# Performance work log

Measured on AMD Instinct MI355X. Metric: run time of the kernel, lower is better.

## Reference

```python
import jax, jax.numpy as jnp
import numpy as np

# Static multi-scale pyramid configuration (matches src_spatial_shapes / level_start_index inputs)
LEVEL_SHAPES = [(128, 128), (64, 64), (32, 32), (16, 16)]  # (H, W) per level
NH, NL, NP = 8, 4, 4  # n_heads, n_levels, n_points
D = 256


def setup_inputs() -> dict:
    key = jax.random.key(0)
    ks = jax.random.split(key, 24)
    N, Lq = 4, 8192
    Lin = sum(h * w for h, w in LEVEL_SHAPES)  # 21760
    d_ff = 4 * D
    inp = {
        "tgt": jax.random.normal(ks[0], (N, Lq, D), jnp.float32),
        "query_pos": jax.random.normal(ks[1], (N, Lq, D), jnp.float32),
        "reference_points": jax.random.uniform(ks[2], (N, Lq, NL, 2), jnp.float32),
        "src": jax.random.normal(ks[3], (N, Lin, D), jnp.float32),
        "src_spatial_shapes": jnp.array(LEVEL_SHAPES, dtype=jnp.int64),
        "level_start_index": jnp.array(np.cumsum([0] + [h * w for h, w in LEVEL_SHAPES[:-1]]), dtype=jnp.int64),
        "src_padding_mask": jnp.zeros((N, Lin), dtype=bool),
        # MSDeformAttn params
        "W_off": jax.random.normal(ks[4], (D, NH * NL * NP * 2), jnp.float32) * 0.01,
        "b_off": jax.random.normal(ks[5], (NH * NL * NP * 2,), jnp.float32) * 0.01,
        "W_attn": jax.random.normal(ks[6], (D, NH * NL * NP), jnp.float32) * 0.02,
        "b_attn": jnp.zeros((NH * NL * NP,), jnp.float32),
        "W_val": jax.random.normal(ks[7], (D, D), jnp.float32) * 0.02,
        "b_val": jnp.zeros((D,), jnp.float32),
        "W_out": jax.random.normal(ks[8], (D, D), jnp.float32) * 0.02,
        "b_out": jnp.zeros((D,), jnp.float32),
        # LN + MLP params
        "ln1_g": jnp.ones((D,), jnp.float32),
        "ln1_b": jnp.zeros((D,), jnp.float32),
        "W_fc1": jax.random.normal(ks[9], (D, d_ff), jnp.float32) * 0.02,
        "b_fc1": jnp.zeros((d_ff,), jnp.float32),
        "W_fc2": jax.random.normal(ks[10], (d_ff, D), jnp.float32) * 0.02,
        "b_fc2": jnp.zeros((D,), jnp.float32),
        "ln2_g": jnp.ones((D,), jnp.float32),
        "ln2_b": jnp.zeros((D,), jnp.float32),
    }
    return inp


def _layer_norm(x, g, b, eps=1e-5):
    x32 = x.astype(jnp.float32)
    m = x32.mean(-1, keepdims=True)
    v = x32.var(-1, keepdims=True)
    return (((x32 - m) * jax.lax.rsqrt(v + eps)) * g + b).astype(x.dtype)


def _sample_level(value_flat, H, W, loc):
    # value_flat: [N, H*W, NH, hd]; loc: [N, Lq, NH, NP, 2] in [0,1]
    # torch.grid_sample align_corners=False, padding_mode='zeros'
    x = loc[..., 0] * W - 0.5
    y = loc[..., 1] * H - 0.5
    x0 = jnp.floor(x)
    y0 = jnp.floor(y)
    dx, dy = x - x0, y - y0
    N, Lq, nh, P = x.shape
    hd = value_flat.shape[-1]
    corners = [
        (x0, y0, (1.0 - dx) * (1.0 - dy)),
        (x0 + 1.0, y0, dx * (1.0 - dy)),
        (x0, y0 + 1.0, (1.0 - dx) * dy),
        (x0 + 1.0, y0 + 1.0, dx * dy),
    ]
    out = jnp.zeros((N, Lq * P, nh, hd), value_flat.dtype)
    for cx, cy, w in corners:
        valid = (cx >= 0) & (cx <= W - 1) & (cy >= 0) & (cy <= H - 1)
        ix = jnp.clip(cx, 0, W - 1).astype(jnp.int32)
        iy = jnp.clip(cy, 0, H - 1).astype(jnp.int32)
        idx = (iy * W + ix).transpose(0, 1, 3, 2).reshape(N, Lq * P, nh)[..., None]
        v = jnp.take_along_axis(value_flat, idx, axis=1)  # [N, Lq*P, NH, hd]
        ww = (w * valid).transpose(0, 1, 3, 2).reshape(N, Lq * P, nh)[..., None]
        out = out + v * ww
    return out.reshape(N, Lq, P, nh, hd)  # [N, Lq, NP, NH, hd]


def reference(tgt, query_pos, reference_points, src, src_spatial_shapes,
              level_start_index, src_padding_mask,
              W_off, b_off, W_attn, b_attn, W_val, b_val, W_out, b_out,
              ln1_g, ln1_b, W_fc1, b_fc1, W_fc2, b_fc2, ln2_g, ln2_b):
    N, Lq, _ = tgt.shape
    hd = D // NH
    q = tgt + query_pos

    # value projection + padding mask
    value = src @ W_val + b_val
    value = jnp.where(src_padding_mask[..., None], 0.0, value)
    value = value.reshape(N, -1, NH, hd)

    # sampling offsets and attention weights
    off = (q @ W_off + b_off).reshape(N, Lq, NH, NL, NP, 2)
    aw = (q @ W_attn + b_attn).reshape(N, Lq, NH, NL * NP)
    aw = jax.nn.softmax(aw, axis=-1).reshape(N, Lq, NH, NL, NP)

    # normalize offsets by (W, H) per level
    normalizer = jnp.array([[w, h] for (h, w) in LEVEL_SHAPES], jnp.float32)  # [NL, 2]
    loc = reference_points[:, :, None, :, None, :] + off / normalizer[None, None, None, :, None, :]

    out = jnp.zeros((N, Lq, NH, hd), value.dtype)
    start = 0
    for l, (H, W) in enumerate(LEVEL_SHAPES):
        vflat = value[:, start:start + H * W]
        start += H * W
        sampled = _sample_level(vflat, H, W, loc[:, :, :, l])  # [N, Lq, NP, NH, hd]
        w_l = aw[:, :, :, l].transpose(0, 1, 3, 2)[..., None]  # [N, Lq, NP, NH, 1]
        out = out + (sampled * w_l).sum(axis=2)
    attn_out = out.reshape(N, Lq, D) @ W_out + b_out

    # residual + LN + MLP (named 'gelu' but is ReLU in source) + LN
    x = _layer_norm(tgt + attn_out, ln1_g, ln1_b)
    h = jax.nn.relu(x @ W_fc1 + b_fc1) @ W_fc2 + b_fc2
    x = _layer_norm(x + h, ln2_g, ln2_b)
    return x
```

## Files before the change

### kernel.cpp

```cpp
#include <hip/hip_runtime.h>
#include <hip/hip_bf16.h>

constexpr int NB    = 4;
constexpr int LQ    = 8192;
constexpr int DM    = 256;
constexpr int NHEAD = 8;
constexpr int HD    = 32;
constexpr int LIN   = 21760;
constexpr int DFF   = 1024;
constexpr int MQ    = NB * LQ;
constexpr int MV    = NB * LIN;

typedef __attribute__((ext_vector_type(8))) short short8;
typedef __attribute__((ext_vector_type(4))) float f32x4;

__device__ __forceinline__ ushort f2b(float f) {
  union { __hip_bfloat16 h; ushort u; } c;
  c.h = __float2bfloat16(f);
  return c.u;
}
__device__ __forceinline__ float b2f(ushort u) {
  return __uint_as_float((unsigned int)u << 16);
}

__device__ __forceinline__ void load_lds16(const ushort* g, ushort* l) {
  __builtin_amdgcn_global_load_lds(
      (const __attribute__((address_space(1))) void*)g,
      (__attribute__((address_space(3))) void*)l, 16, 0, 0);
}

__global__ __launch_bounds__(256) void k_packall(
    const float* __restrict__ Wval, const float* __restrict__ Woff,
    const float* __restrict__ Wattn, const float* __restrict__ Wout,
    const float* __restrict__ W1, const float* __restrict__ W2,
    ushort* __restrict__ wvalP, ushort* __restrict__ wqP,
    ushort* __restrict__ woutP, ushort* __restrict__ w1P,
    ushort* __restrict__ w2P) {
  const int bid = blockIdx.x;
  const float* W; ushort* P; int K, Nsrc, n_base, local;
  if (bid < 64)       { W = Wval;  P = wvalP; K = 256;  Nsrc = 256;  n_base = 0;   local = bid; }
  else if (bid < 128) { W = Woff;  P = wqP;   K = 256;  Nsrc = 256;  n_base = 0;   local = bid - 64; }
  else if (bid < 160) { W = Wattn; P = wqP;   K = 256;  Nsrc = 128;  n_base = 256; local = bid - 128; }
  else if (bid < 224) { W = Wout;  P = woutP; K = 256;  Nsrc = 256;  n_base = 0;   local = bid - 160; }
  else if (bid < 480) { W = W1;    P = w1P;   K = 256;  Nsrc = 1024; n_base = 0;   local = bid - 224; }
  else                { W = W2;    P = w2P;   K = 1024; Nsrc = 256;  n_base = 0;   local = bid - 480; }
  const int kb = local % (K >> 5), nb = local / (K >> 5);
  const int k0 = kb * 32, n0 = nb * 32;

  __shared__ float T[32][33];
  const int t = threadIdx.x;
  {
    const int r = t >> 3, c4 = t & 7;
    const float4 v = *reinterpret_cast<const float4*>(
        &W[(size_t)(k0 + r) * Nsrc + n0 + c4 * 4]);
    T[r][c4 * 4 + 0] = v.x;
    T[r][c4 * 4 + 1] = v.y;
    T[r][c4 * 4 + 2] = v.z;
    T[r][c4 * 4 + 3] = v.w;
  }
  __syncthreads();
  const int dn = t >> 3, q = t & 7;
  const int n = n_base + n0 + dn;
  const int k = k0 + q * 4;
  const int Tt = n >> 4, fr = n & 15, kg = (k >> 3) & 3;
  const int idx = Tt * (K >> 5) + (k >> 5);
  ushort4 o;
  o.x = f2b(T[q * 4 + 0][dn]);
  o.y = f2b(T[q * 4 + 1][dn]);
  o.z = f2b(T[q * 4 + 2][dn]);
  o.w = f2b(T[q * 4 + 3][dn]);
  *reinterpret_cast<ushort4*>(&P[(size_t)idx * 512 + (kg * 16 + fr) * 8 + (k & 7)]) = o;
}

template<int MODE, int ASRC>
__global__ __launch_bounds__(256) void k_gemm(
    const void* __restrict__ Ap, const float* __restrict__ A2,
    const ushort* __restrict__ BP,
    const float* __restrict__ bias,
    void* __restrict__ out0, int M, int N, int K) {
  __shared__ __align__(16) ushort SMEM[17408];
  ushort* As = SMEM;
  const int m0 = blockIdx.x * 128, n0 = blockIdx.y * 128;
  const int t = threadIdx.x, w = t >> 6, l = t & 63;
  const int wr = (w >> 1) * 64, wc = (w & 1) * 64;
  const int fr = l & 15, kg = l >> 4;
  const int lrow = l >> 3;
  const int sg = (l & 7) ^ lrow;
  const int Kg = K >> 5;

  f32x4 acc[4][4];
#pragma unroll
  for (int i = 0; i < 4; ++i)
#pragma unroll
    for (int j = 0; j < 4; ++j) acc[i][j] = f32x4{0.f, 0.f, 0.f, 0.f};

  const float* Af = (const float*)Ap;

  for (int k0 = 0; k0 < K; k0 += 64) {
    float4 fa[4][2];
#pragma unroll
    for (int i = 0; i < 4; ++i) {
      const float* ap = Af + (size_t)(m0 + i * 32 + w * 8 + lrow) * K + k0 + sg * 8;
      fa[i][0] = *reinterpret_cast<const float4*>(ap);
      fa[i][1] = *reinterpret_cast<const float4*>(ap + 4);
      if constexpr (ASRC == 2) {
        const float* ap2 = A2 + (size_t)(m0 + i * 32 + w * 8 + lrow) * K + k0 + sg * 8;
        const float4 x = *reinterpret_cast<const float4*>(ap2);
        const float4 y = *reinterpret_cast<const float4*>(ap2 + 4);
        fa[i][0].x += x.x; fa[i][0].y += x.y; fa[i][0].z += x.z; fa[i][0].w += x.w;
        fa[i][1].x += y.x; fa[i][1].y += y.y; fa[i][1].z += y.z; fa[i][1].w += y.w;
      }
    }
    __syncthreads();
#pragma unroll
    for (int i = 0; i < 4; ++i) {
      uint4 u;
      u.x = (unsigned int)f2b(fa[i][0].x) | ((unsigned int)f2b(fa[i][0].y) << 16);
      u.y = (unsigned int)f2b(fa[i][0].z) | ((unsigned int)f2b(fa[i][0].w) << 16);
      u.z = (unsigned int)f2b(fa[i][1].x) | ((unsigned int)f2b(fa[i][1].y) << 16);
      u.w = (unsigned int)f2b(fa[i][1].z) | ((unsigned int)f2b(fa[i][1].w) << 16);
      *reinterpret_cast<uint4*>(As + i * 2048 + w * 512 + l * 8) = u;
    }
    __syncthreads();
#pragma unroll
    for (int kk = 0; kk < 2; ++kk) {
      short8 a[4], b[4];
#pragma unroll
      for (int i = 0; i < 4; ++i)
        a[i] = *reinterpret_cast<const short8*>(
            &As[(wr + i * 16 + fr) * 64 + ((kk * 4 + kg) ^ (fr & 7)) * 8]);
#pragma unroll
      for (int i = 0; i < 4; ++i)
        b[i] = *reinterpret_cast<const short8*>(
            BP + ((size_t)((n0 >> 4) + (w & 1) * 4 + i) * Kg + (k0 >> 5) + kk) * 512 + l * 8);
#pragma unroll
      for (int mi = 0; mi < 4; ++mi)
#pragma unroll
        for (int ni = 0; ni < 4; ++ni)
          acc[mi][ni] = __builtin_amdgcn_mfma_f32_16x16x32_bf16(
              b[ni], a[mi], acc[mi][ni], 0, 0, 0);
    }
  }

  ushort (*LC)[136] = (ushort(*)[136])SMEM;
  __syncthreads();
#pragma unroll
  for (int ni = 0; ni < 4; ++ni) {
    const float4 bv = *reinterpret_cast<const float4*>(&bias[n0 + wc + ni * 16 + kg * 4]);
#pragma unroll
    for (int mi = 0; mi < 4; ++mi) {
      ushort4 p;
      p.x = f2b(acc[mi][ni][0] + bv.x);
      p.y = f2b(acc[mi][ni][1] + bv.y);
      p.z = f2b(acc[mi][ni][2] + bv.z);
      p.w = f2b(acc[mi][ni][3] + bv.w);
      *reinterpret_cast<ushort4*>(&LC[wr + mi * 16 + fr][wc + ni * 16 + kg * 4]) = p;
    }
  }
  __syncthreads();
  const int c = t & 15, rb = t >> 4;
#pragma unroll
  for (int i = 0; i < 8; ++i) {
    const int r = rb + i * 16;
    const uint4 vv = *reinterpret_cast<const uint4*>(&LC[r][c * 8]);
    *reinterpret_cast<uint4*>((ushort*)out0 + (size_t)(m0 + r) * N + n0 + c * 8) = vv;
  }
}

__global__ __launch_bounds__(256) void k_qlogit(
    const float* __restrict__ tgt, const float* __restrict__ qpos,
    const ushort* __restrict__ BP, const float* __restrict__ battn,
    float* __restrict__ awb) {
  __shared__ __align__(16) ushort SMEM[17408];
  ushort* As = SMEM;
  const int m0 = blockIdx.x * 128;
  const int t = threadIdx.x, w = t >> 6, l = t & 63;
  const int wc = (w & 1) * 64;
  const int fr = l & 15, kg = l >> 4;
  const int lrow = l >> 3;
  const int sg = (l & 7) ^ lrow;

  f32x4 acc[4][4];
#pragma unroll
  for (int i = 0; i < 4; ++i)
#pragma unroll
    for (int j = 0; j < 4; ++j) acc[i][j] = f32x4{0.f, 0.f, 0.f, 0.f};

  for (int k0 = 0; k0 < 256; k0 += 64) {
    float4 fa[4][2];
#pragma unroll
    for (int i = 0; i < 4; ++i) {
      const float* ap = tgt + (size_t)(m0 + i * 32 + w * 8 + lrow) * 256 + k0 + sg * 8;
      const float* ap2 = qpos + (size_t)(m0 + i * 32 + w * 8 + lrow) * 256 + k0 + sg * 8;
      fa[i][0] = *reinterpret_cast<const float4*>(ap);
      fa[i][1] = *reinterpret_cast<const float4*>(ap + 4);
      const float4 x = *reinterpret_cast<const float4*>(ap2);
      const float4 y = *reinterpret_cast<const float4*>(ap2 + 4);
      fa[i][0].x += x.x; fa[i][0].y += x.y; fa[i][0].z += x.z; fa[i][0].w += x.w;
      fa[i][1].x += y.x; fa[i][1].y += y.y; fa[i][1].z += y.z; fa[i][1].w += y.w;
    }
    __syncthreads();
#pragma unroll
    for (int i = 0; i < 4; ++i) {
      uint4 u;
      u.x = (unsigned int)f2b(fa[i][0].x) | ((unsigned int)f2b(fa[i][0].y) << 16);
      u.y = (unsigned int)f2b(fa[i][0].z) | ((unsigned int)f2b(fa[i][0].w) << 16);
      u.z = (unsigned int)f2b(fa[i][1].x) | ((unsigned int)f2b(fa[i][1].y) << 16);
      u.w = (unsigned int)f2b(fa[i][1].z) | ((unsigned int)f2b(fa[i][1].w) << 16);
      *reinterpret_cast<uint4*>(As + i * 2048 + w * 512 + l * 8) = u;
    }
    __syncthreads();
#pragma unroll
    for (int kk = 0; kk < 2; ++kk) {
      short8 a[4], b[4];
#pragma unroll
      for (int i = 0; i < 4; ++i)
        a[i] = *reinterpret_cast<const short8*>(
            &As[((w >> 1) * 64 + i * 16 + fr) * 64 + ((kk * 4 + kg) ^ (fr & 7)) * 8]);
#pragma unroll
      for (int i = 0; i < 4; ++i)
        b[i] = *reinterpret_cast<const short8*>(
            BP + ((size_t)(16 + (w & 1) * 4 + i) * 8 + (k0 >> 5) + kk) * 512 + l * 8);
#pragma unroll
      for (int mi = 0; mi < 4; ++mi)
#pragma unroll
        for (int ni = 0; ni < 4; ++ni)
          acc[mi][ni] = __builtin_amdgcn_mfma_f32_16x16x32_bf16(
              b[ni], a[mi], acc[mi][ni], 0, 0, 0);
    }
  }

  float (*LF)[132] = (float(*)[132])SMEM;
#pragma unroll
  for (int p = 0; p < 2; ++p) {
    __syncthreads();
    if ((w >> 1) == p) {
#pragma unroll
      for (int ni = 0; ni < 4; ++ni) {
        const float4 bv = *reinterpret_cast<const float4*>(&battn[wc + ni * 16 + kg * 4]);
#pragma unroll
        for (int mi = 0; mi < 4; ++mi) {
          float4 v;
          v.x = acc[mi][ni][0] + bv.x; v.y = acc[mi][ni][1] + bv.y;
          v.z = acc[mi][ni][2] + bv.z; v.w = acc[mi][ni][3] + bv.w;
          *reinterpret_cast<float4*>(&LF[mi * 16 + fr][wc + ni * 16 + kg * 4]) = v;
        }
      }
    }
    __syncthreads();
#pragma unroll
    for (int gi = 0; gi < 2; ++gi) {
      const int g = t + gi * 256;
      const int row = g >> 3, hh = g & 7;
      const float* src = &LF[row][hh * 16];
      float e[16];
      float4 v0 = *reinterpret_cast<const float4*>(src);
      float4 v1 = *reinterpret_cast<const float4*>(src + 4);
      float4 v2 = *reinterpret_cast<const float4*>(src + 8);
      float4 v3 = *reinterpret_cast<const float4*>(src + 12);
      e[0]=v0.x; e[1]=v0.y; e[2]=v0.z; e[3]=v0.w;
      e[4]=v1.x; e[5]=v1.y; e[6]=v1.z; e[7]=v1.w;
      e[8]=v2.x; e[9]=v2.y; e[10]=v2.z; e[11]=v2.w;
      e[12]=v3.x; e[13]=v3.y; e[14]=v3.z; e[15]=v3.w;
      float mx = e[0];
#pragma unroll
      for (int i = 1; i < 16; ++i) mx = fmaxf(mx, e[i]);
      float s = 0.f;
#pragma unroll
      for (int i = 0; i < 16; ++i) { e[i] = __expf(e[i] - mx); s += e[i]; }
      const float inv = 1.f / s;
      float* o = awb + (size_t)(m0 + p * 64 + row) * 128 + hh * 16;
      float4 q;
      q.x = e[0]*inv; q.y = e[1]*inv; q.z = e[2]*inv; q.w = e[3]*inv;
      *reinterpret_cast<float4*>(o) = q;
      q.x = e[4]*inv; q.y = e[5]*inv; q.z = e[6]*inv; q.w = e[7]*inv;
      *reinterpret_cast<float4*>(o + 4) = q;
      q.x = e[8]*inv; q.y = e[9]*inv; q.z = e[10]*inv; q.w = e[11]*inv;
      *reinterpret_cast<float4*>(o + 8) = q;
      q.x = e[12]*inv; q.y = e[13]*inv; q.z = e[14]*inv; q.w = e[15]*inv;
      *reinterpret_cast<float4*>(o + 12) = q;
    }
  }
}

__global__ __launch_bounds__(256) void k_outln(
    const ushort* __restrict__ A, const ushort* __restrict__ BP,
    const float* __restrict__ bias, const float* __restrict__ res,
    const float* __restrict__ g, const float* __restrict__ bvec,
    ushort* __restrict__ out, int K) {
  __shared__ __align__(16) ushort SMEM[17408];
  ushort* As = SMEM;
  const int m0 = blockIdx.x * 64;
  const int t = threadIdx.x, w = t >> 6, l = t & 63;
  const int wc = w * 64;
  const int fr = l & 15, kg = l >> 4;
  const int lrow = l >> 3;
  const int sg = (l & 7) ^ lrow;
  const int Kg = K >> 5;

  f32x4 acc[4][4];
#pragma unroll
  for (int i = 0; i < 4; ++i)
#pragma unroll
    for (int j = 0; j < 4; ++j) acc[i][j] = f32x4{0.f, 0.f, 0.f, 0.f};

  for (int k0 = 0; k0 < K; k0 += 64) {
    __syncthreads();
#pragma unroll
    for (int i = 0; i < 2; ++i)
      load_lds16(A + (size_t)(m0 + i * 32 + w * 8 + lrow) * K + k0 + sg * 8,
                 As + i * 2048 + w * 512);
    __syncthreads();
#pragma unroll
    for (int kk = 0; kk < 2; ++kk) {
      short8 a[4], b[4];
#pragma unroll
      for (int i = 0; i < 4; ++i)
        a[i] = *reinterpret_cast<const short8*>(
            &As[(i * 16 + fr) * 64 + ((kk * 4 + kg) ^ (fr & 7)) * 8]);
#pragma unroll
      for (int i = 0; i < 4; ++i)
        b[i] = *reinterpret_cast<const short8*>(
            BP + ((size_t)(w * 4 + i) * Kg + (k0 >> 5) + kk) * 512 + l * 8);
#pragma unroll
      for (int mi = 0; mi < 4; ++mi)
#pragma unroll
        for (int ni = 0; ni < 4; ++ni)
          acc[mi][ni] = __builtin_amdgcn_mfma_f32_16x16x32_bf16(
              b[ni], a[mi], acc[mi][ni], 0, 0, 0);
    }
  }

  ushort (*LY)[272] = (ushort(*)[272])SMEM;
  __syncthreads();
#pragma unroll
  for (int ni = 0; ni < 4; ++ni) {
    const float4 bv = *reinterpret_cast<const float4*>(&bias[wc + ni * 16 + kg * 4]);
#pragma unroll
    for (int mi = 0; mi < 4; ++mi) {
      ushort4 p;
      p.x = f2b(acc[mi][ni][0] + bv.x);
      p.y = f2b(acc[mi][ni][1] + bv.y);
      p.z = f2b(acc[mi][ni][2] + bv.z);
      p.w = f2b(acc[mi][ni][3] + bv.w);
      *reinterpret_cast<ushort4*>(&LY[mi * 16 + fr][wc + ni * 16 + kg * 4]) = p;
    }
  }
  __syncthreads();

  const int c = t & 31, rb = t >> 5;
#pragma unroll
  for (int i = 0; i < 8; ++i) {
    const int r = rb + i * 8;
    const uint4 yy = *reinterpret_cast<const uint4*>(&LY[r][c * 8]);
    const unsigned int yw[4] = {yy.x, yy.y, yy.z, yy.w};
    float v[8];
#pragma unroll
    for (int j = 0; j < 4; ++j) {
      v[2 * j]     = __uint_as_float(yw[j] << 16);
      v[2 * j + 1] = __uint_as_float(yw[j] & 0xffff0000u);
    }
    const float* rp = res + (size_t)(m0 + r) * 256 + c * 8;
    const float4 r0 = *reinterpret_cast<const float4*>(rp);
    const float4 r1 = *reinterpret_cast<const float4*>(rp + 4);
    v[0] += r0.x; v[1] += r0.y; v[2] += r0.z; v[3] += r0.w;
    v[4] += r1.x; v[5] += r1.y; v[6] += r1.z; v[7] += r1.w;
    float s = 0.f, ss = 0.f;
#pragma unroll
    for (int j = 0; j < 8; ++j) { s += v[j]; ss += v[j] * v[j]; }
#pragma unroll
    for (int o = 1; o < 32; o <<= 1) {
      s  += __shfl_xor(s, o);
      ss += __shfl_xor(ss, o);
    }
    const float m = s * (1.f / 256.f);
    const float inv = rsqrtf(ss * (1.f / 256.f) - m * m + 1e-5f);
    const float4 g0 = *reinterpret_cast<const float4*>(&g[c * 8]);
    const float4 g1 = *reinterpret_cast<const float4*>(&g[c * 8 + 4]);
    const float4 b0 = *reinterpret_cast<const float4*>(&bvec[c * 8]);
    const float4 b1 = *reinterpret_cast<const float4*>(&bvec[c * 8 + 4]);
    uint4 u;
    u.x = (unsigned int)f2b((v[0] - m) * inv * g0.x + b0.x) |
          ((unsigned int)f2b((v[1] - m) * inv * g0.y + b0.y) << 16);
    u.y = (unsigned int)f2b((v[2] - m) * inv * g0.z + b0.z) |
          ((unsigned int)f2b((v[3] - m) * inv * g0.w + b0.w) << 16);
    u.z = (unsigned int)f2b((v[4] - m) * inv * g1.x + b1.x) |
          ((unsigned int)f2b((v[5] - m) * inv * g1.y + b1.y) << 16);
    u.w = (unsigned int)f2b((v[6] - m) * inv * g1.z + b1.z) |
          ((unsigned int)f2b((v[7] - m) * inv * g1.w + b1.w) << 16);
    *reinterpret_cast<uint4*>(out + (size_t)(m0 + r) * 256 + c * 8) = u;
  }
}

__global__ __launch_bounds__(256) void k_ffn(
    const ushort* __restrict__ X, const ushort* __restrict__ W1P,
    const float* __restrict__ bb1, const ushort* __restrict__ W2P,
    const float* __restrict__ bb2, const float* __restrict__ g2,
    const float* __restrict__ b2v, float* __restrict__ out) {
  __shared__ __align__(16) ushort SMEM[24576];
  ushort* Xs = SMEM;
  ushort* Hs = SMEM + 16384;
  const int m0 = blockIdx.x * 64;
  const int t = threadIdx.x, w = t >> 6, l = t & 63;
  const int fr = l & 15, kg = l >> 4;

#pragma unroll
  for (int i = 0; i < 8; ++i) {
    const int gi = w * 8 + i;
    const int row = gi * 2 + (l >> 5);
    load_lds16(X + (size_t)(m0 + row) * 256 + (((l & 31) ^ (row & 7)) * 8),
               Xs + gi * 512);
  }
  __syncthreads();

  f32x4 acc2[4][4];
#pragma unroll
  for (int i = 0; i < 4; ++i)
#pragma unroll
    for (int j = 0; j < 4; ++j) acc2[i][j] = f32x4{0.f, 0.f, 0.f, 0.f};

  for (int c = 0; c < 8; ++c) {
    f32x4 acc1[4][2];
#pragma unroll
    for (int i = 0; i < 4; ++i)
#pragma unroll
      for (int j = 0; j < 2; ++j) acc1[i][j] = f32x4{0.f, 0.f, 0.f, 0.f};
#pragma unroll
    for (int ks = 0; ks < 8; ++ks) {
      short8 a[4], b[2];
#pragma unroll
      for (int mi = 0; mi < 4; ++mi)
        a[mi] = *reinterpret_cast<const short8*>(
            &Xs[(mi * 16 + fr) * 256 + ((ks * 4 + kg) ^ (fr & 7)) * 8]);
#pragma unroll
      for (int ni = 0; ni < 2; ++ni)
        b[ni] = *reinterpret_cast<const short8*>(
            W1P + ((size_t)(c * 8 + w * 2 + ni) * 8 + ks) * 512 + l * 8);
#pragma unroll
      for (int mi = 0; mi < 4; ++mi)
#pragma unroll
        for (int ni = 0; ni < 2; ++ni)
          acc1[mi][ni] = __builtin_amdgcn_mfma_f32_16x16x32_bf16(
              b[ni], a[mi], acc1[mi][ni], 0, 0, 0);
    }
    __syncthreads();
#pragma unroll
    for (int ni = 0; ni < 2; ++ni) {
      const float4 bv = *reinterpret_cast<const float4*>(
          &bb1[c * 128 + w * 32 + ni * 16 + kg * 4]);
#pragma unroll
      for (int mi = 0; mi < 4; ++mi) {
        const int row = mi * 16 + fr;
        const int gcol = w * 4 + ni * 2 + (kg >> 1);
        ushort4 p;
        p.x = f2b(fmaxf(acc1[mi][ni][0] + bv.x, 0.f));
        p.y = f2b(fmaxf(acc1[mi][ni][1] + bv.y, 0.f));
        p.z = f2b(fmaxf(acc1[mi][ni][2] + bv.z, 0.f));
        p.w = f2b(fmaxf(acc1[mi][ni][3] + bv.w, 0.f));
        *reinterpret_cast<ushort4*>(
            &Hs[row * 128 + ((gcol ^ (fr & 7)) * 8) + (kg & 1) * 4]) = p;
      }
    }
    __syncthreads();
#pragma unroll
    for (int ks2 = 0; ks2 < 4; ++ks2) {
      short8 a2[4], b2[4];
#pragma unroll
      for (int mi = 0; mi < 4; ++mi)
        a2[mi] = *reinterpret_cast<const short8*>(
            &Hs[(mi * 16 + fr) * 128 + ((ks2 * 4 + kg) ^ (fr & 7)) * 8]);
#pragma unroll
      for (int ni = 0; ni < 4; ++ni)
        b2[ni] = *reinterpret_cast<const short8*>(
            W2P + ((size_t)(w * 4 + ni) * 32 + c * 4 + ks2) * 512 + l * 8);
#pragma unroll
      for (int mi = 0; mi < 4; ++mi)
#pragma unroll
        for (int ni = 0; ni < 4; ++ni)
          acc2[mi][ni] = __builtin_amdgcn_mfma_f32_16x16x32_bf16(
              b2[ni], a2[mi], acc2[mi][ni], 0, 0, 0);
    }
  }

#pragma unroll
  for (int ni = 0; ni < 4; ++ni) {
    const int colb = w * 64 + ni * 16 + kg * 4;
    const float4 bv = *reinterpret_cast<const float4*>(&bb2[colb]);
    const int g = w * 8 + ni * 2 + (kg >> 1);
#pragma unroll
    for (int mi = 0; mi < 4; ++mi) {
      const int row = mi * 16 + fr;
      const ushort4 xr = *reinterpret_cast<const ushort4*>(
          &Xs[row * 256 + ((g ^ (fr & 7)) * 8) + (kg & 1) * 4]);
      acc2[mi][ni][0] += bv.x + b2f(xr.x);
      acc2[mi][ni][1] += bv.y + b2f(xr.y);
      acc2[mi][ni][2] += bv.z + b2f(xr.z);
      acc2[mi][ni][3] += bv.w + b2f(xr.w);
    }
  }
  __syncthreads();

  ushort (*LY)[272] = (ushort(*)[272])SMEM;
#pragma unroll
  for (int ni = 0; ni < 4; ++ni) {
#pragma unroll
    for (int mi = 0; mi < 4; ++mi) {
      ushort4 p;
      p.x = f2b(acc2[mi][ni][0]);
      p.y = f2b(acc2[mi][ni][1]);
      p.z = f2b(acc2[mi][ni][2]);
      p.w = f2b(acc2[mi][ni][3]);
      *reinterpret_cast<ushort4*>(&LY[mi * 16 + fr][w * 64 + ni * 16 + kg * 4]) = p;
    }
  }
  __syncthreads();

  const int cc = t & 31, rb = t >> 5;
#pragma unroll
  for (int i = 0; i < 8; ++i) {
    const int r = rb + i * 8;
    const uint4 yy = *reinterpret_cast<const uint4*>(&LY[r][cc * 8]);
    const unsigned int yw[4] = {yy.x, yy.y, yy.z, yy.w};
    float v[8];
#pragma unroll
    for (int j = 0; j < 4; ++j) {
      v[2 * j]     = __uint_as_float(yw[j] << 16);
      v[2 * j + 1] = __uint_as_float(yw[j] & 0xffff0000u);
    }
    float s = 0.f, ss = 0.f;
#pragma unroll
    for (int j = 0; j < 8; ++j) { s += v[j]; ss += v[j] * v[j]; }
#pragma unroll
    for (int o = 1; o < 32; o <<= 1) {
      s  += __shfl_xor(s, o);
      ss += __shfl_xor(ss, o);
    }
    const float m = s * (1.f / 256.f);
    const float inv = rsqrtf(ss * (1.f / 256.f) - m * m + 1e-5f);
    const float4 g0 = *reinterpret_cast<const float4*>(&g2[cc * 8]);
    const float4 g1 = *reinterpret_cast<const float4*>(&g2[cc * 8 + 4]);
    const float4 b0 = *reinterpret_cast<const float4*>(&b2v[cc * 8]);
    const float4 b1 = *reinterpret_cast<const float4*>(&b2v[cc * 8 + 4]);
    float* opp = out + (size_t)(m0 + r) * 256 + cc * 8;
    float4 q0, q1;
    q0.x = (v[0] - m) * inv * g0.x + b0.x;
    q0.y = (v[1] - m) * inv * g0.y + b0.y;
    q0.z = (v[2] - m) * inv * g0.z + b0.z;
    q0.w = (v[3] - m) * inv * g0.w + b0.w;
    q1.x = (v[4] - m) * inv * g1.x + b1.x;
    q1.y = (v[5] - m) * inv * g1.y + b1.y;
    q1.z = (v[6] - m) * inv * g1.z + b1.z;
    q1.w = (v[7] - m) * inv * g1.w + b1.w;
    *reinterpret_cast<float4*>(opp) = q0;
    *reinterpret_cast<float4*>(opp + 4) = q1;
  }
}

__global__ __launch_bounds__(256) void k_sample(
    const float* __restrict__ refp, const ushort* __restrict__ offb,
    const float* __restrict__ awb, const ushort* __restrict__ value,
    ushort* __restrict__ pre) {
  const int bid = ((blockIdx.x & 7) << 9) | (blockIdx.x >> 3);
  const int tid = bid * 256 + threadIdx.x;
  const int cg = tid & 3;
  const int h  = (tid >> 2) & 7;
  const int nq = tid >> 5;
  const int n  = nq >> 13;

  const float4 r01 = *reinterpret_cast<const float4*>(refp + (size_t)nq * 8);
  const float4 r23 = *reinterpret_cast<const float4*>(refp + (size_t)nq * 8 + 4);
  const float rxs[4] = {r01.x, r01.z, r23.x, r23.z};
  const float rys[4] = {r01.y, r01.w, r23.y, r23.w};
  const ushort* op = offb + (size_t)nq * 256 + h * 32;
  const float*  ap = awb + (size_t)nq * 128 + h * 16;
  const ushort* vb = value + (size_t)n * LIN * DM + h * HD + cg * 8;

  float acc[8];
#pragma unroll
  for (int j = 0; j < 8; ++j) acc[j] = 0.f;

  const int WL[4] = {128, 64, 32, 16};
  const int ST[4] = {0, 16384, 20480, 21504};

#pragma unroll
  for (int lvl = 0; lvl < 4; ++lvl) {
    const int Wl = WL[lvl];
    const float fW = (float)Wl;
    const float invW = 1.f / fW;
    const float rx = rxs[lvl], ry = rys[lvl];
    const ushort* vl = vb + (size_t)ST[lvl] * DM;
    const uint4 ov = *reinterpret_cast<const uint4*>(op + lvl * 8);
    const float4 a4 = *reinterpret_cast<const float4*>(ap + lvl * 4);
    const unsigned int ow[4] = {ov.x, ov.y, ov.z, ov.w};
    const float aa[4] = {a4.x, a4.y, a4.z, a4.w};
#pragma unroll
    for (int p = 0; p < 4; ++p) {
      const float ox = __uint_as_float(ow[p] << 16);
      const float oy = __uint_as_float(ow[p] & 0xffff0000u);
      const float xx = (rx + ox * invW) * fW - 0.5f;
      const float yy = (ry + oy * invW) * fW - 0.5f;
      const float a = aa[p];
      const float x0 = floorf(xx), y0 = floorf(yy);
      const float dx = xx - x0, dy = yy - y0;
      const bool vx0 = (x0 >= 0.f) && (x0 <= fW - 1.f);
      const bool vx1 = (x0 + 1.f >= 0.f) && (x0 + 1.f <= fW - 1.f);
      const bool vy0 = (y0 >= 0.f) && (y0 <= fW - 1.f);
      const bool vy1 = (y0 + 1.f >= 0.f) && (y0 + 1.f <= fW - 1.f);
      const int ix0 = min(max((int)x0, 0), Wl - 1);
      const int ix1 = min(max((int)x0 + 1, 0), Wl - 1);
      const int iy0 = min(max((int)y0, 0), Wl - 1);
      const int iy1 = min(max((int)y0 + 1, 0), Wl - 1);
      const float w00 = (vx0 && vy0) ? (1.f - dx) * (1.f - dy) * a : 0.f;
      const float w10 = (vx1 && vy0) ? dx * (1.f - dy) * a : 0.f;
      const float w01 = (vx0 && vy1) ? (1.f - dx) * dy * a : 0.f;
      const float w11 = (vx1 && vy1) ? dx * dy * a : 0.f;
      const ushort* r0 = vl + (size_t)iy0 * Wl * DM;
      const ushort* r1 = vl + (size_t)iy1 * Wl * DM;
      const uint4 u00 = *reinterpret_cast<const uint4*>(r0 + ix0 * DM);
      const uint4 u10 = *reinterpret_cast<const uint4*>(r0 + ix1 * DM);
      const uint4 u01 = *reinterpret_cast<const uint4*>(r1 + ix0 * DM);
      const uint4 u11 = *reinterpret_cast<const uint4*>(r1 + ix1 * DM);
      const unsigned int uu00[4] = {u00.x, u00.y, u00.z, u00.w};
      const unsigned int uu10[4] = {u10.x, u10.y, u10.z, u10.w};
      const unsigned int uu01[4] = {u01.x, u01.y, u01.z, u01.w};
      const unsigned int uu11[4] = {u11.x, u11.y, u11.z, u11.w};
#pragma unroll
      for (int i = 0; i < 4; ++i) {
        acc[2 * i]     += __uint_as_float(uu00[i] << 16) * w00;
        acc[2 * i + 1] += __uint_as_float(uu00[i] & 0xffff0000u) * w00;
        acc[2 * i]     += __uint_as_float(uu10[i] << 16) * w10;
        acc[2 * i + 1] += __uint_as_float(uu10[i] & 0xffff0000u) * w10;
        acc[2 * i]     += __uint_as_float(uu01[i] << 16) * w01;
        acc[2 * i + 1] += __uint_as_float(uu01[i] & 0xffff0000u) * w01;
        acc[2 * i]     += __uint_as_float(uu11[i] << 16) * w11;
        acc[2 * i + 1] += __uint_as_float(uu11[i] & 0xffff0000u) * w11;
      }
    }
  }

  uint4 o;
  o.x = (unsigned int)f2b(acc[0]) | ((unsigned int)f2b(acc[1]) << 16);
  o.y = (unsigned int)f2b(acc[2]) | ((unsigned int)f2b(acc[3]) << 16);
  o.z = (unsigned int)f2b(acc[4]) | ((unsigned int)f2b(acc[5]) << 16);
  o.w = (unsigned int)f2b(acc[6]) | ((unsigned int)f2b(acc[7]) << 16);
  *reinterpret_cast<uint4*>(pre + (size_t)nq * DM + h * HD + cg * 8) = o;
}

extern "C" void kernel_launch(void* const* d_in, const int* in_sizes, int n_in,
                              void* d_out, int out_size, void* d_ws, size_t ws_size,
                              hipStream_t stream) {
  const float* tgt   = (const float*)d_in[0];
  const float* qpos  = (const float*)d_in[1];
  const float* refp  = (const float*)d_in[2];
  const float* src   = (const float*)d_in[3];
  const float* Woff  = (const float*)d_in[7];
  const float* boff  = (const float*)d_in[8];
  const float* Wattn = (const float*)d_in[9];
  const float* battn = (const float*)d_in[10];
  const float* Wval  = (const float*)d_in[11];
  const float* bval  = (const float*)d_in[12];
  const float* Wout  = (const float*)d_in[13];
  const float* bout  = (const float*)d_in[14];
  const float* g1    = (const float*)d_in[15];
  const float* b1    = (const float*)d_in[16];
  const float* W1    = (const float*)d_in[17];
  const float* bb1   = (const float*)d_in[18];
  const float* W2    = (const float*)d_in[19];
  const float* bb2   = (const float*)d_in[20];
  const float* g2    = (const float*)d_in[21];
  const float* b2v   = (const float*)d_in[22];
  float* out = (float*)d_out;

  char* ws = (char*)d_ws;
  ushort* offb   = (ushort*)(ws + 0);
  ushort* valueb = (ushort*)(ws + 44564480);
  ushort* preb   = (ushort*)(ws + 89128960);
  float*  awb    = (float*)(ws + 105906176);
  ushort* xb     = (ushort*)(ws + 0);
  ushort* wvalP  = (ushort*)(ws + 156237824);
  ushort* wqP    = wvalP + 65536;
  ushort* woutP  = wqP + 98304;
  ushort* w1P    = woutP + 65536;
  ushort* w2P    = w1P + 262144;

  hipLaunchKernelGGL(k_packall, dim3(736), dim3(256), 0, stream,
                     Wval, Woff, Wattn, Wout, W1, W2,
                     wvalP, wqP, woutP, w1P, w2P);

  hipLaunchKernelGGL((k_gemm<0, 1>), dim3(MV / 128, 2), dim3(256), 0, stream,
                     (const void*)src, (const float*)nullptr, wvalP, bval,
                     (void*)valueb, MV, DM, DM);

  hipLaunchKernelGGL((k_gemm<0, 2>), dim3(MQ / 128, 2), dim3(256), 0, stream,
                     (const void*)tgt, qpos, wqP, boff,
                     (void*)offb, MQ, DM, DM);

  hipLaunchKernelGGL(k_qlogit, dim3(MQ / 128), dim3(256), 0, stream,
                     tgt, qpos, wqP, battn, awb);

  hipLaunchKernelGGL(k_sample, dim3(MQ * NHEAD * 4 / 256), dim3(256), 0, stream,
                     refp, offb, awb, valueb, preb);

  hipLaunchKernelGGL(k_outln, dim3(MQ / 64), dim3(256), 0, stream,
                     preb, woutP, bout, tgt, g1, b1, xb, DM);

  hipLaunchKernelGGL(k_ffn, dim3(MQ / 64), dim3(256), 0, stream,
                     xb, w1P, bb1, w2P, bb2, g2, b2v, out);
}
```

Measured before the change: 219.9 us.

## Store value tensor head-major and remap sampler blocks to one head per block

The value-projection GEMM gets a new output mode that writes the value tensor as [N, head, pixel, 32] instead of [N, pixel, 256], so each head's pixels sit contiguously. The sampling kernel is remapped so each block handles 64 queries of a single (batch, head) pair, and bilinear gathers index into the compact per-head plane. This aims to improve cache locality for the random bilinear gathers, since one block now only touches that head's slice of the value tensor. The GEMM epilogue gains per-row division and scattered 16-byte stores, and the adjacent-thread access pattern in the sampler changes.

```diff
diff --git a/kernel.cpp b/kernel.cpp
--- a/kernel.cpp
+++ b/kernel.cpp
@@ -163,7 +163,17 @@
   for (int i = 0; i < 8; ++i) {
     const int r = rb + i * 16;
     const uint4 vv = *reinterpret_cast<const uint4*>(&LC[r][c * 8]);
-    *reinterpret_cast<uint4*>((ushort*)out0 + (size_t)(m0 + r) * N + n0 + c * 8) = vv;
+    if constexpr (MODE == 0) {
+      *reinterpret_cast<uint4*>((ushort*)out0 + (size_t)(m0 + r) * N + n0 + c * 8) = vv;
+    } else {
+      const int row = m0 + r;
+      const int n = row / LIN;
+      const int pix = row - n * LIN;
+      const int col = n0 + c * 8;
+      const int h = col >> 5, ch = col & 31;
+      *reinterpret_cast<uint4*>((ushort*)out0 +
+          (((size_t)(n * NHEAD + h) * LIN + pix) * 32 + ch)) = vv;
+    }
   }
 }
 
@@ -560,12 +570,12 @@
     const float* __restrict__ refp, const ushort* __restrict__ offb,
     const float* __restrict__ awb, const ushort* __restrict__ value,
     ushort* __restrict__ pre) {
-  const int bid = ((blockIdx.x & 7) << 9) | (blockIdx.x >> 3);
-  const int tid = bid * 256 + threadIdx.x;
-  const int cg = tid & 3;
-  const int h  = (tid >> 2) & 7;
-  const int nq = tid >> 5;
-  const int n  = nq >> 13;
+  const int work = ((blockIdx.x & 7) << 9) | (blockIdx.x >> 3);
+  const int nh = work >> 7;
+  const int n = nh >> 3, h = nh & 7;
+  const int t = threadIdx.x;
+  const int cg = t & 3, qi = t >> 2;
+  const int nq = n * LQ + (work & 127) * 64 + qi;
 
   const float4 r01 = *reinterpret_cast<const float4*>(refp + (size_t)nq * 8);
   const float4 r23 = *reinterpret_cast<const float4*>(refp + (size_t)nq * 8 + 4);
@@ -573,7 +583,7 @@
   const float rys[4] = {r01.y, r01.w, r23.y, r23.w};
   const ushort* op = offb + (size_t)nq * 256 + h * 32;
   const float*  ap = awb + (size_t)nq * 128 + h * 16;
-  const ushort* vb = value + (size_t)n * LIN * DM + h * HD + cg * 8;
+  const ushort* vb = value + (size_t)nh * LIN * 32 + cg * 8;
 
   float acc[8];
 #pragma unroll
@@ -588,7 +598,7 @@
     const float fW = (float)Wl;
     const float invW = 1.f / fW;
     const float rx = rxs[lvl], ry = rys[lvl];
-    const ushort* vl = vb + (size_t)ST[lvl] * DM;
+    const ushort* vl = vb + (size_t)ST[lvl] * 32;
     const uint4 ov = *reinterpret_cast<const uint4*>(op + lvl * 8);
     const float4 a4 = *reinterpret_cast<const float4*>(ap + lvl * 4);
     const unsigned int ow[4] = {ov.x, ov.y, ov.z, ov.w};
@@ -614,12 +624,12 @@
       const float w10 = (vx1 && vy0) ? dx * (1.f - dy) * a : 0.f;
       const float w01 = (vx0 && vy1) ? (1.f - dx) * dy * a : 0.f;
       const float w11 = (vx1 && vy1) ? dx * dy * a : 0.f;
-      const ushort* r0 = vl + (size_t)iy0 * Wl * DM;
-      const ushort* r1 = vl + (size_t)iy1 * Wl * DM;
-      const uint4 u00 = *reinterpret_cast<const uint4*>(r0 + ix0 * DM);
-      const uint4 u10 = *reinterpret_cast<const uint4*>(r0 + ix1 * DM);
-      const uint4 u01 = *reinterpret_cast<const uint4*>(r1 + ix0 * DM);
-      const uint4 u11 = *reinterpret_cast<const uint4*>(r1 + ix1 * DM);
+      const ushort* r0 = vl + (size_t)iy0 * Wl * 32;
+      const ushort* r1 = vl + (size_t)iy1 * Wl * 32;
+      const uint4 u00 = *reinterpret_cast<const uint4*>(r0 + ix0 * 32);
+      const uint4 u10 = *reinterpret_cast<const uint4*>(r0 + ix1 * 32);
+      const uint4 u01 = *reinterpret_cast<const uint4*>(r1 + ix0 * 32);
+      const uint4 u11 = *reinterpret_cast<const uint4*>(r1 + ix1 * 32);
       const unsigned int uu00[4] = {u00.x, u00.y, u00.z, u00.w};
       const unsigned int uu10[4] = {u10.x, u10.y, u10.z, u10.w};
       const unsigned int uu01[4] = {u01.x, u01.y, u01.z, u01.w};
@@ -643,7 +653,7 @@
   o.y = (unsigned int)f2b(acc[2]) | ((unsigned int)f2b(acc[3]) << 16);
   o.z = (unsigned int)f2b(acc[4]) | ((unsigned int)f2b(acc[5]) << 16);
   o.w = (unsigned int)f2b(acc[6]) | ((unsigned int)f2b(acc[7]) << 16);
-  *reinterpret_cast<uint4*>(pre + (size_t)nq * DM + h * HD + cg * 8) = o;
+  *reinterpret_cast<uint4*>(pre + (size_t)nq * 256 + h * 32 + cg * 8) = o;
 }
 
 extern "C" void kernel_launch(void* const* d_in, const int* in_sizes, int n_in,
@@ -687,7 +697,7 @@
                      Wval, Woff, Wattn, Wout, W1, W2,
                      wvalP, wqP, woutP, w1P, w2P);
 
-  hipLaunchKernelGGL((k_gemm<0, 1>), dim3(MV / 128, 2), dim3(256), 0, stream,
+  hipLaunchKernelGGL((k_gemm<4, 1>), dim3(MV / 128, 2), dim3(256), 0, stream,
                      (const void*)src, (const float*)nullptr, wvalP, bval,
                      (void*)valueb, MV, DM, DM);
 
```

After: 242.3 us. +10.2%, slower.

## Fuse sampling-offset GEMM and attention-logit softmax into one query projection kernel

Applied to the files above, without the earlier changes.

Replaces the separate offset GEMM and attention-logit kernel with a single kernel that computes all 384 output columns (256 offsets plus 128 logits) from one load of tgt+query_pos per 64-row tile. Each wave handles 96 columns, and the epilogue writes the bf16 offsets and a softmaxed weight buffer in three staged passes through shared memory. This removes a second read of tgt and qpos and one launch. In exchange, the logits are now rounded to bf16 before the softmax, which slightly reduces their precision, and the kernel holds a larger per-thread accumulator set.

```diff
diff --git a/kernel.cpp b/kernel.cpp
--- a/kernel.cpp
+++ b/kernel.cpp
@@ -72,12 +72,10 @@
   *reinterpret_cast<ushort4*>(&P[(size_t)idx * 512 + (kg * 16 + fr) * 8 + (k & 7)]) = o;
 }
 
-template<int MODE, int ASRC>
-__global__ __launch_bounds__(256) void k_gemm(
-    const void* __restrict__ Ap, const float* __restrict__ A2,
-    const ushort* __restrict__ BP,
+__global__ __launch_bounds__(256) void k_gemmA(
+    const float* __restrict__ Af, const ushort* __restrict__ BP,
     const float* __restrict__ bias,
-    void* __restrict__ out0, int M, int N, int K) {
+    ushort* __restrict__ out0, int M, int N, int K) {
   __shared__ __align__(16) ushort SMEM[17408];
   ushort* As = SMEM;
   const int m0 = blockIdx.x * 128, n0 = blockIdx.y * 128;
@@ -94,8 +92,6 @@
 #pragma unroll
     for (int j = 0; j < 4; ++j) acc[i][j] = f32x4{0.f, 0.f, 0.f, 0.f};
 
-  const float* Af = (const float*)Ap;
-
   for (int k0 = 0; k0 < K; k0 += 64) {
     float4 fa[4][2];
 #pragma unroll
@@ -103,13 +99,6 @@
       const float* ap = Af + (size_t)(m0 + i * 32 + w * 8 + lrow) * K + k0 + sg * 8;
       fa[i][0] = *reinterpret_cast<const float4*>(ap);
       fa[i][1] = *reinterpret_cast<const float4*>(ap + 4);
-      if constexpr (ASRC == 2) {
-        const float* ap2 = A2 + (size_t)(m0 + i * 32 + w * 8 + lrow) * K + k0 + sg * 8;
-        const float4 x = *reinterpret_cast<const float4*>(ap2);
-        const float4 y = *reinterpret_cast<const float4*>(ap2 + 4);
-        fa[i][0].x += x.x; fa[i][0].y += x.y; fa[i][0].z += x.z; fa[i][0].w += x.w;
-        fa[i][1].x += y.x; fa[i][1].y += y.y; fa[i][1].z += y.z; fa[i][1].w += y.w;
-      }
     }
     __syncthreads();
 #pragma unroll
@@ -163,35 +152,37 @@
   for (int i = 0; i < 8; ++i) {
     const int r = rb + i * 16;
     const uint4 vv = *reinterpret_cast<const uint4*>(&LC[r][c * 8]);
-    *reinterpret_cast<uint4*>((ushort*)out0 + (size_t)(m0 + r) * N + n0 + c * 8) = vv;
-  }
-}
-
-__global__ __launch_bounds__(256) void k_qlogit(
+    *reinterpret_cast<uint4*>(out0 + (size_t)(m0 + r) * N + n0 + c * 8) = vv;
+  }
+}
+
+__global__ __launch_bounds__(256) void k_qproj(
     const float* __restrict__ tgt, const float* __restrict__ qpos,
-    const ushort* __restrict__ BP, const float* __restrict__ battn,
-    float* __restrict__ awb) {
-  __shared__ __align__(16) ushort SMEM[17408];
+    const ushort* __restrict__ BP, const float* __restrict__ boff,
+    const float* __restrict__ battn,
+    ushort* __restrict__ offb, float* __restrict__ awb) {
+  __shared__ __align__(16) ushort SMEM[8704];
+  __shared__ __align__(16) ushort LY[64][136];
   ushort* As = SMEM;
-  const int m0 = blockIdx.x * 128;
+  const int m0 = blockIdx.x * 64;
   const int t = threadIdx.x, w = t >> 6, l = t & 63;
-  const int wc = (w & 1) * 64;
   const int fr = l & 15, kg = l >> 4;
   const int lrow = l >> 3;
   const int sg = (l & 7) ^ lrow;
 
-  f32x4 acc[4][4];
+  f32x4 acc[4][6];
 #pragma unroll
   for (int i = 0; i < 4; ++i)
 #pragma unroll
-    for (int j = 0; j < 4; ++j) acc[i][j] = f32x4{0.f, 0.f, 0.f, 0.f};
+    for (int j = 0; j < 6; ++j) acc[i][j] = f32x4{0.f, 0.f, 0.f, 0.f};
 
   for (int k0 = 0; k0 < 256; k0 += 64) {
-    float4 fa[4][2];
-#pragma unroll
-    for (int i = 0; i < 4; ++i) {
-      const float* ap = tgt + (size_t)(m0 + i * 32 + w * 8 + lrow) * 256 + k0 + sg * 8;
-      const float* ap2 = qpos + (size_t)(m0 + i * 32 + w * 8 + lrow) * 256 + k0 + sg * 8;
+    float4 fa[2][2];
+#pragma unroll
+    for (int i = 0; i < 2; ++i) {
+      const int row = m0 + i * 32 + w * 8 + lrow;
+      const float* ap = tgt + (size_t)row * 256 + k0 + sg * 8;
+      const float* ap2 = qpos + (size_t)row * 256 + k0 + sg * 8;
       fa[i][0] = *reinterpret_cast<const float4*>(ap);
       fa[i][1] = *reinterpret_cast<const float4*>(ap + 4);
       const float4 x = *reinterpret_cast<const float4*>(ap2);
@@ -201,7 +192,7 @@
     }
     __syncthreads();
 #pragma unroll
-    for (int i = 0; i < 4; ++i) {
+    for (int i = 0; i < 2; ++i) {
       uint4 u;
       u.x = (unsigned int)f2b(fa[i][0].x) | ((unsigned int)f2b(fa[i][0].y) << 16);
       u.y = (unsigned int)f2b(fa[i][0].z) | ((unsigned int)f2b(fa[i][0].w) << 16);
@@ -212,73 +203,86 @@
     __syncthreads();
 #pragma unroll
     for (int kk = 0; kk < 2; ++kk) {
-      short8 a[4], b[4];
+      short8 a[4], b[6];
 #pragma unroll
       for (int i = 0; i < 4; ++i)
         a[i] = *reinterpret_cast<const short8*>(
-            &As[((w >> 1) * 64 + i * 16 + fr) * 64 + ((kk * 4 + kg) ^ (fr & 7)) * 8]);
-#pragma unroll
-      for (int i = 0; i < 4; ++i)
+            &As[(i * 16 + fr) * 64 + ((kk * 4 + kg) ^ (fr & 7)) * 8]);
+#pragma unroll
+      for (int i = 0; i < 6; ++i)
         b[i] = *reinterpret_cast<const short8*>(
-            BP + ((size_t)(16 + (w & 1) * 4 + i) * 8 + (k0 >> 5) + kk) * 512 + l * 8);
+            BP + ((size_t)(w * 6 + i) * 8 + (k0 >> 5) + kk) * 512 + l * 8);
 #pragma unroll
       for (int mi = 0; mi < 4; ++mi)
 #pragma unroll
-        for (int ni = 0; ni < 4; ++ni)
+        for (int ni = 0; ni < 6; ++ni)
           acc[mi][ni] = __builtin_amdgcn_mfma_f32_16x16x32_bf16(
               b[ni], a[mi], acc[mi][ni], 0, 0, 0);
     }
   }
 
-  float (*LF)[132] = (float(*)[132])SMEM;
-#pragma unroll
-  for (int p = 0; p < 2; ++p) {
-    __syncthreads();
-    if ((w >> 1) == p) {
-#pragma unroll
-      for (int ni = 0; ni < 4; ++ni) {
-        const float4 bv = *reinterpret_cast<const float4*>(&battn[wc + ni * 16 + kg * 4]);
+#pragma unroll
+  for (int p = 0; p < 3; ++p) {
+    __syncthreads();
+#pragma unroll
+    for (int ni = 0; ni < 6; ++ni) {
+      const int cb = w * 96 + ni * 16;
+      if (cb >= p * 128 && cb < p * 128 + 128) {
+        const int col = cb + kg * 4;
+        float4 bv;
+        if (col < 256) bv = *reinterpret_cast<const float4*>(&boff[col]);
+        else           bv = *reinterpret_cast<const float4*>(&battn[col - 256]);
 #pragma unroll
         for (int mi = 0; mi < 4; ++mi) {
-          float4 v;
-          v.x = acc[mi][ni][0] + bv.x; v.y = acc[mi][ni][1] + bv.y;
-          v.z = acc[mi][ni][2] + bv.z; v.w = acc[mi][ni][3] + bv.w;
-          *reinterpret_cast<float4*>(&LF[mi * 16 + fr][wc + ni * 16 + kg * 4]) = v;
+          ushort4 q;
+          q.x = f2b(acc[mi][ni][0] + bv.x);
+          q.y = f2b(acc[mi][ni][1] + bv.y);
+          q.z = f2b(acc[mi][ni][2] + bv.z);
+          q.w = f2b(acc[mi][ni][3] + bv.w);
+          *reinterpret_cast<ushort4*>(&LY[mi * 16 + fr][cb - p * 128 + kg * 4]) = q;
         }
       }
     }
     __syncthreads();
-#pragma unroll
-    for (int gi = 0; gi < 2; ++gi) {
-      const int g = t + gi * 256;
-      const int row = g >> 3, hh = g & 7;
-      const float* src = &LF[row][hh * 16];
-      float e[16];
-      float4 v0 = *reinterpret_cast<const float4*>(src);
-      float4 v1 = *reinterpret_cast<const float4*>(src + 4);
-      float4 v2 = *reinterpret_cast<const float4*>(src + 8);
-      float4 v3 = *reinterpret_cast<const float4*>(src + 12);
-      e[0]=v0.x; e[1]=v0.y; e[2]=v0.z; e[3]=v0.w;
-      e[4]=v1.x; e[5]=v1.y; e[6]=v1.z; e[7]=v1.w;
-      e[8]=v2.x; e[9]=v2.y; e[10]=v2.z; e[11]=v2.w;
-      e[12]=v3.x; e[13]=v3.y; e[14]=v3.z; e[15]=v3.w;
-      float mx = e[0];
-#pragma unroll
-      for (int i = 1; i < 16; ++i) mx = fmaxf(mx, e[i]);
-      float s = 0.f;
-#pragma unroll
-      for (int i = 0; i < 16; ++i) { e[i] = __expf(e[i] - mx); s += e[i]; }
-      const float inv = 1.f / s;
-      float* o = awb + (size_t)(m0 + p * 64 + row) * 128 + hh * 16;
-      float4 q;
-      q.x = e[0]*inv; q.y = e[1]*inv; q.z = e[2]*inv; q.w = e[3]*inv;
-      *reinterpret_cast<float4*>(o) = q;
-      q.x = e[4]*inv; q.y = e[5]*inv; q.z = e[6]*inv; q.w = e[7]*inv;
-      *reinterpret_cast<float4*>(o + 4) = q;
-      q.x = e[8]*inv; q.y = e[9]*inv; q.z = e[10]*inv; q.w = e[11]*inv;
-      *reinterpret_cast<float4*>(o + 8) = q;
-      q.x = e[12]*inv; q.y = e[13]*inv; q.z = e[14]*inv; q.w = e[15]*inv;
-      *reinterpret_cast<float4*>(o + 12) = q;
+    if (p < 2) {
+      const int c = t & 15, rb = t >> 4;
+#pragma unroll
+      for (int i = 0; i < 4; ++i) {
+        const int r = rb + i * 16;
+        const uint4 vv = *reinterpret_cast<const uint4*>(&LY[r][c * 8]);
+        *reinterpret_cast<uint4*>(offb + (size_t)(m0 + r) * 256 + p * 128 + c * 8) = vv;
+      }
+    } else {
+#pragma unroll
+      for (int gi = 0; gi < 2; ++gi) {
+        const int g = t + gi * 256;
+        const int row = g >> 3, hh = g & 7;
+        const uint4 u0 = *reinterpret_cast<const uint4*>(&LY[row][hh * 16]);
+        const uint4 u1 = *reinterpret_cast<const uint4*>(&LY[row][hh * 16 + 8]);
+        const unsigned int uw[8] = {u0.x, u0.y, u0.z, u0.w, u1.x, u1.y, u1.z, u1.w};
+        float e[16];
+#pragma unroll
+        for (int i = 0; i < 4; ++i) {
+          e[2*i]   = __uint_as_float(uw[i] << 16);
+          e[2*i+1] = __uint_as_float(uw[i] & 0xffff0000u);
+          e[8+2*i]   = __uint_as_float(uw[4+i] << 16);
+          e[8+2*i+1] = __uint_as_float(uw[4+i] & 0xffff0000u);
+        }
+        float mx = e[0];
+#pragma unroll
+        for (int i = 1; i < 16; ++i) mx = fmaxf(mx, e[i]);
+        float s = 0.f;
+#pragma unroll
+        for (int i = 0; i < 16; ++i) { e[i] = __expf(e[i] - mx); s += e[i]; }
+        const float inv = 1.f / s;
+        float* o = awb + (size_t)(m0 + row) * 128 + hh * 16;
+#pragma unroll
+        for (int i = 0; i < 4; ++i) {
+          float4 q;
+          q.x = e[4*i]*inv; q.y = e[4*i+1]*inv; q.z = e[4*i+2]*inv; q.w = e[4*i+3]*inv;
+          *reinterpret_cast<float4*>(o + 4*i) = q;
+        }
+      }
     }
   }
 }
@@ -687,16 +691,11 @@
                      Wval, Woff, Wattn, Wout, W1, W2,
                      wvalP, wqP, woutP, w1P, w2P);
 
-  hipLaunchKernelGGL((k_gemm<0, 1>), dim3(MV / 128, 2), dim3(256), 0, stream,
-                     (const void*)src, (const float*)nullptr, wvalP, bval,
-                     (void*)valueb, MV, DM, DM);
-
-  hipLaunchKernelGGL((k_gemm<0, 2>), dim3(MQ / 128, 2), dim3(256), 0, stream,
-                     (const void*)tgt, qpos, wqP, boff,
-                     (void*)offb, MQ, DM, DM);
-
-  hipLaunchKernelGGL(k_qlogit, dim3(MQ / 128), dim3(256), 0, stream,
-                     tgt, qpos, wqP, battn, awb);
+  hipLaunchKernelGGL(k_gemmA, dim3(MV / 128, 2), dim3(256), 0, stream,
+                     src, wvalP, bval, valueb, MV, DM, DM);
+
+  hipLaunchKernelGGL(k_qproj, dim3(MQ / 64), dim3(256), 0, stream,
+                     tgt, qpos, wqP, boff, battn, offb, awb);
 
   hipLaunchKernelGGL(k_sample, dim3(MQ * NHEAD * 4 / 256), dim3(256), 0, stream,
                      refp, offb, awb, valueb, preb);
```

Result: no change. 216.1 us, median of 2 (-1.7%).
